# Optimization experiments

Hardware: AMD Instinct MI355X
Metric: run time of the kernel (lower is better)

Reference implementation:

```python
import jax, jax.numpy as jnp
import numpy as np

E, N, D, H = 16, 2048, 1024, 4096

def setup_inputs() -> dict:
    key = jax.random.key(0)
    k1, k2, k3 = jax.random.split(key, 3)
    x = jax.random.normal(k1, (E, N, D), dtype=jnp.float32)
    # init_tensor in the repo is Kaiming-style uniform init; use uniform(-1/sqrt(fan_in), 1/sqrt(fan_in))
    s1 = 1.0 / np.sqrt(D)
    s2 = 1.0 / np.sqrt(H)
    w1 = jax.random.uniform(k2, (E, D, H), dtype=jnp.float32, minval=-s1, maxval=s1)
    w2 = jax.random.uniform(k3, (E, H, D), dtype=jnp.float32, minval=-s2, maxval=s2)
    return {"x": x, "w1": w1, "w2": w2}

def reference(x, w1, w2):
    # per-expert 2-layer MLP: grouped GEMM -> GELU -> grouped GEMM
    hidden = jnp.einsum('end,edh->enh', x, w1)
    hidden = jax.nn.gelu(hidden, approximate=False)  # torch nn.GELU default (erf)
    out = jnp.einsum('enh,ehd->end', hidden, w2)
    return out
```

## Files before the change

kernel.cpp:

```cpp
#include <hip/hip_runtime.h>
#include <stdint.h>
#include <math.h>

#define E_    16
#define NTOK  2048
#define D_    1024
#define H_    4096

typedef unsigned short ushort_t;
typedef __attribute__((ext_vector_type(8))) short short8;
typedef __attribute__((ext_vector_type(4))) float f32x4;

__device__ __forceinline__ ushort_t f2bf(float f) {
    union { float f; unsigned int u; } v; v.f = f;
    unsigned int u = v.u;
    return (ushort_t)((u + 0x7FFFu + ((u >> 16) & 1u)) >> 16);
}

__device__ __forceinline__ void async_copy16(const ushort_t* g, ushort_t* l) {
    __builtin_amdgcn_global_load_lds(
        (const __attribute__((address_space(1))) void*)g,
        (__attribute__((address_space(3))) void*)l,
        16, 0, 0);
}


__global__ void cvt_f32_bf16(const float* __restrict__ in, ushort_t* __restrict__ out) {
    int i = blockIdx.x * blockDim.x + threadIdx.x;
    const float4 v = *(const float4*)(in + (size_t)i * 4);
    ushort4 o;
    o.x = f2bf(v.x); o.y = f2bf(v.y); o.z = f2bf(v.z); o.w = f2bf(v.w);
    *(ushort4*)(out + (size_t)i * 4) = o;
}

__global__ void transpose_cvt(const float* __restrict__ in, ushort_t* __restrict__ out,
                              int R, int C) {
    __shared__ float tile[64][65];
    const int e = blockIdx.z;
    const float*  inp  = in  + (size_t)e * R * C;
    ushort_t*     outp = out + (size_t)e * R * C;
    const int c0 = blockIdx.x * 64, r0 = blockIdx.y * 64;
    const int tx = threadIdx.x & 63, ty = threadIdx.x >> 6;
    #pragma unroll
    for (int i = 0; i < 16; ++i) {
        int r = ty * 16 + i;
        tile[r][tx] = inp[(size_t)(r0 + r) * C + c0 + tx];
    }
    __syncthreads();
    #pragma unroll
    for (int i = 0; i < 16; ++i) {
        int c = ty * 16 + i;
        outp[(size_t)(c0 + c) * R + r0 + tx] = f2bf(tile[tx][c]);
    }
}


template<bool GELU, typename CT>
__global__ void gemm_bt(const ushort_t* __restrict__ A, const ushort_t* __restrict__ Bt,
                        CT* __restrict__ C, int M, int N, int K) {
    __shared__ ushort_t As[128 * 64];
    __shared__ ushort_t Bs[128 * 64];

    const int e  = blockIdx.z;
    const int bm = blockIdx.y, bn = blockIdx.x;
    const ushort_t* Ae = A  + (size_t)e * M * K + (size_t)(bm * 128) * K;
    const ushort_t* Be = Bt + (size_t)e * N * K + (size_t)(bn * 128) * K;
    CT* Ce = C + (size_t)e * M * N;

    const int tid  = threadIdx.x;
    const int wave = tid >> 6, lane = tid & 63;
    const int wm = wave & 1, wn = wave >> 1;
    const int lr = lane & 15;
    const int lk = (lane >> 4) * 8;

    f32x4 acc[4][4];
    #pragma unroll
    for (int i = 0; i < 4; ++i)
        #pragma unroll
        for (int j = 0; j < 4; ++j)
            acc[i][j] = (f32x4)(0.0f);

    const int row_s = lane >> 3;
    const int ch    = (lane & 7) * 8;

    const int KT = K >> 6;
    for (int kt = 0; kt < KT; ++kt) {
        const int k0 = kt * 64;
        #pragma unroll
        for (int t = 0; t < 4; ++t) {
            const int rb = (wave * 4 + t) * 8;
            async_copy16(Ae + (size_t)(rb + row_s) * K + k0 + ch, &As[rb * 64]);
            async_copy16(Be + (size_t)(rb + row_s) * K + k0 + ch, &Bs[rb * 64]);
        }
        __syncthreads();

        #pragma unroll
        for (int kk = 0; kk < 2; ++kk) {
            short8 a[4], b[4];
            #pragma unroll
            for (int i = 0; i < 4; ++i)
                a[i] = *(const short8*)&As[(wm * 64 + i * 16 + lr) * 64 + kk * 32 + lk];
            #pragma unroll
            for (int j = 0; j < 4; ++j)
                b[j] = *(const short8*)&Bs[(wn * 64 + j * 16 + lr) * 64 + kk * 32 + lk];
            #pragma unroll
            for (int i = 0; i < 4; ++i)
                #pragma unroll
                for (int j = 0; j < 4; ++j)
                    acc[i][j] = __builtin_amdgcn_mfma_f32_16x16x32_bf16(
                        a[i], b[j], acc[i][j], 0, 0, 0);
        }
        __syncthreads();
    }

    const int cr = (lane >> 4) * 4;
    const int cc = lane & 15;
    #pragma unroll
    for (int i = 0; i < 4; ++i) {
        #pragma unroll
        for (int j = 0; j < 4; ++j) {
            #pragma unroll
            for (int r = 0; r < 4; ++r) {
                const int row = bm * 128 + wm * 64 + i * 16 + cr + r;
                const int col = bn * 128 + wn * 64 + j * 16 + cc;
                float v = acc[i][j][r];
                if constexpr (GELU) {
                    v = 0.5f * v * (1.0f + erff(v * 0.70710678118654752f));
                    Ce[(size_t)row * N + col] = (CT)f2bf(v);
                } else {
                    Ce[(size_t)row * N + col] = v;
                }
            }
        }
    }
}


extern "C" void kernel_launch(void* const* d_in, const int* in_sizes, int n_in,
                              void* d_out, int out_size, void* d_ws, size_t ws_size,
                              hipStream_t stream) {
    const float* x  = (const float*)d_in[0];
    const float* w1 = (const float*)d_in[1];
    const float* w2 = (const float*)d_in[2];
    float* out = (float*)d_out;

    ushort_t* xb  = (ushort_t*)d_ws;
    ushort_t* w1t = xb  + (size_t)E_ * NTOK * D_;
    ushort_t* w2t = w1t + (size_t)E_ * D_ * H_;
    ushort_t* hid = w2t + (size_t)E_ * H_ * D_;

    {
        const size_t n = (size_t)E_ * NTOK * D_;
        cvt_f32_bf16<<<dim3((unsigned)(n / 4 / 256)), dim3(256), 0, stream>>>(x, xb);
    }
    transpose_cvt<<<dim3(H_ / 64, D_ / 64, E_), dim3(256), 0, stream>>>(w1, w1t, D_, H_);
    transpose_cvt<<<dim3(D_ / 64, H_ / 64, E_), dim3(256), 0, stream>>>(w2, w2t, H_, D_);

    gemm_bt<true, ushort_t><<<dim3(H_ / 128, NTOK / 128, E_), dim3(256), 0, stream>>>(
        xb, w1t, hid, NTOK, H_, D_);

    gemm_bt<false, float><<<dim3(D_ / 128, NTOK / 128, E_), dim3(256), 0, stream>>>(
        hid, w2t, out, NTOK, D_, H_);
}
```

Before: 1.335 ms.

## Swizzle GEMM LDS layout, stage GELU output through LDS, vectorize transposes

The GEMM's LDS tiles now use an XOR swizzle on the 16-byte chunk index, applied both in the async global-to-LDS copy and in the MFMA operand reads, to cut LDS bank conflicts. The GELU epilogue writes bf16 results into a padded LDS buffer first, then stores them to global memory as coalesced 16-byte rows instead of scattered 2-byte stores. The weight transpose kernels now use float4 loads and ushort4 stores. These changes add an extra barrier and LDS round-trip in the first GEMM epilogue, and the LDS buffer for the GELU variant grows slightly.

```diff
diff --git a/kernel.cpp b/kernel.cpp
--- a/kernel.cpp
+++ b/kernel.cpp
@@ -40,17 +40,22 @@
     const float*  inp  = in  + (size_t)e * R * C;
     ushort_t*     outp = out + (size_t)e * R * C;
     const int c0 = blockIdx.x * 64, r0 = blockIdx.y * 64;
-    const int tx = threadIdx.x & 63, ty = threadIdx.x >> 6;
+    const int tx = threadIdx.x & 15, ty = threadIdx.x >> 4;
     #pragma unroll
-    for (int i = 0; i < 16; ++i) {
-        int r = ty * 16 + i;
-        tile[r][tx] = inp[(size_t)(r0 + r) * C + c0 + tx];
+    for (int i = 0; i < 4; ++i) {
+        const int r = i * 16 + ty;
+        const float4 v = *(const float4*)(inp + (size_t)(r0 + r) * C + c0 + tx * 4);
+        tile[r][tx * 4 + 0] = v.x; tile[r][tx * 4 + 1] = v.y;
+        tile[r][tx * 4 + 2] = v.z; tile[r][tx * 4 + 3] = v.w;
     }
     __syncthreads();
     #pragma unroll
-    for (int i = 0; i < 16; ++i) {
-        int c = ty * 16 + i;
-        outp[(size_t)(c0 + c) * R + r0 + tx] = f2bf(tile[tx][c]);
+    for (int i = 0; i < 4; ++i) {
+        const int c = i * 16 + ty;
+        ushort4 o;
+        o.x = f2bf(tile[tx * 4 + 0][c]); o.y = f2bf(tile[tx * 4 + 1][c]);
+        o.z = f2bf(tile[tx * 4 + 2][c]); o.w = f2bf(tile[tx * 4 + 3][c]);
+        *(ushort4*)(outp + (size_t)(c0 + c) * R + r0 + tx * 4) = o;
     }
 }
 
@@ -58,8 +63,10 @@
 template<bool GELU, typename CT>
 __global__ void gemm_bt(const ushort_t* __restrict__ A, const ushort_t* __restrict__ Bt,
                         CT* __restrict__ C, int M, int N, int K) {
-    __shared__ ushort_t As[128 * 64];
-    __shared__ ushort_t Bs[128 * 64];
+    constexpr int SMEM_USH = GELU ? (128 * 130) : (128 * 64 * 2);
+    __shared__ ushort_t smem[SMEM_USH];
+    ushort_t* As = smem;
+    ushort_t* Bs = smem + 128 * 64;
 
     const int e  = blockIdx.z;
     const int bm = blockIdx.y, bn = blockIdx.x;
@@ -71,7 +78,8 @@
     const int wave = tid >> 6, lane = tid & 63;
     const int wm = wave & 1, wn = wave >> 1;
     const int lr = lane & 15;
-    const int lk = (lane >> 4) * 8;
+    const int h  = lr & 7;
+    const int cq = lane >> 4;
 
     f32x4 acc[4][4];
     #pragma unroll
@@ -81,7 +89,7 @@
             acc[i][j] = (f32x4)(0.0f);
 
     const int row_s = lane >> 3;
-    const int ch    = (lane & 7) * 8;
+    const int ch    = ((lane & 7) ^ row_s) * 8;
 
     const int KT = K >> 6;
     for (int kt = 0; kt < KT; ++kt) {
@@ -99,10 +107,12 @@
             short8 a[4], b[4];
             #pragma unroll
             for (int i = 0; i < 4; ++i)
-                a[i] = *(const short8*)&As[(wm * 64 + i * 16 + lr) * 64 + kk * 32 + lk];
+                a[i] = *(const short8*)&As[(wm * 64 + i * 16 + lr) * 64 +
+                                           (((kk * 4 + cq) ^ h) << 3)];
             #pragma unroll
             for (int j = 0; j < 4; ++j)
-                b[j] = *(const short8*)&Bs[(wn * 64 + j * 16 + lr) * 64 + kk * 32 + lk];
+                b[j] = *(const short8*)&Bs[(wn * 64 + j * 16 + lr) * 64 +
+                                           (((kk * 4 + cq) ^ h) << 3)];
             #pragma unroll
             for (int i = 0; i < 4; ++i)
                 #pragma unroll
@@ -115,23 +125,43 @@
 
     const int cr = (lane >> 4) * 4;
     const int cc = lane & 15;
-    #pragma unroll
-    for (int i = 0; i < 4; ++i) {
+
+    if constexpr (GELU) {
         #pragma unroll
-        for (int j = 0; j < 4; ++j) {
+        for (int i = 0; i < 4; ++i)
             #pragma unroll
-            for (int r = 0; r < 4; ++r) {
-                const int row = bm * 128 + wm * 64 + i * 16 + cr + r;
-                const int col = bn * 128 + wn * 64 + j * 16 + cc;
-                float v = acc[i][j][r];
-                if constexpr (GELU) {
+            for (int j = 0; j < 4; ++j)
+                #pragma unroll
+                for (int r = 0; r < 4; ++r) {
+                    const int row = wm * 64 + i * 16 + cr + r;
+                    const int col = wn * 64 + j * 16 + cc;
+                    float v = acc[i][j][r];
                     v = 0.5f * v * (1.0f + erff(v * 0.70710678118654752f));
-                    Ce[(size_t)row * N + col] = (CT)f2bf(v);
-                } else {
-                    Ce[(size_t)row * N + col] = v;
+                    smem[row * 130 + col] = f2bf(v);
                 }
-            }
+        __syncthreads();
+        const unsigned int* p32 = (const unsigned int*)smem;
+        const int rty = tid >> 4, rtx = tid & 15;
+        #pragma unroll
+        for (int it = 0; it < 8; ++it) {
+            const int row = it * 16 + rty;
+            const int base = row * 65 + rtx * 4;
+            uint4 v;
+            v.x = p32[base + 0]; v.y = p32[base + 1];
+            v.z = p32[base + 2]; v.w = p32[base + 3];
+            *(uint4*)(Ce + (size_t)(bm * 128 + row) * N + bn * 128 + rtx * 8) = v;
         }
+    } else {
+        #pragma unroll
+        for (int i = 0; i < 4; ++i)
+            #pragma unroll
+            for (int j = 0; j < 4; ++j)
+                #pragma unroll
+                for (int r = 0; r < 4; ++r) {
+                    const int row = bm * 128 + wm * 64 + i * 16 + cr + r;
+                    const int col = bn * 128 + wn * 64 + j * 16 + cc;
+                    Ce[(size_t)row * N + col] = acc[i][j][r];
+                }
     }
 }
 
```

Result: faster. 1.295 ms (-2.9%).
